# Kernel tuning notes

Hardware: AMD Instinct MI355X
Metric: run time of the kernel (lower is better)

## Reference

```python
import jax, jax.numpy as jnp
import numpy as np

B, S, D = 4, 2048, 768
H = 12
HD = D // H  # 64


def setup_inputs() -> dict:
    key = jax.random.key(0)
    k1, k2, k3 = jax.random.split(key, 3)
    x = jax.random.normal(k1, (B, S, D), dtype=jnp.float32)
    w_qkv = jax.random.normal(k2, (D, 3 * D), dtype=jnp.float32) * (1.0 / np.sqrt(D))
    b_qkv = jnp.zeros((3 * D,), dtype=jnp.float32)
    w_proj = jax.random.normal(k3, (D, D), dtype=jnp.float32) * (1.0 / np.sqrt(D))
    b_proj = jnp.zeros((D,), dtype=jnp.float32)
    return {"x": x, "w_qkv": w_qkv, "b_qkv": b_qkv, "w_proj": w_proj, "b_proj": b_proj}


def reference(x, w_qkv, b_qkv, w_proj, b_proj):
    b, s, d = x.shape
    qkv = x @ w_qkv + b_qkv                      # [B,S,3D]
    q, k, v = jnp.split(qkv, 3, axis=-1)
    # [B,S,D] -> [B,H,S,HD]
    q = q.reshape(b, s, H, HD).transpose(0, 2, 1, 3)
    k = k.reshape(b, s, H, HD).transpose(0, 2, 1, 3)
    v = v.reshape(b, s, H, HD).transpose(0, 2, 1, 3)
    scores = jnp.einsum("bhqd,bhkd->bhqk", q, k) / jnp.sqrt(jnp.float32(HD))
    causal = jnp.tril(jnp.ones((s, s), dtype=bool))
    scores = jnp.where(causal[None, None, :, :], scores, jnp.float32(-jnp.inf))
    attn = jax.nn.softmax(scores, axis=-1)       # dropout p=0.0 -> identity
    out = jnp.einsum("bhqk,bhkd->bhqd", attn, v)  # [B,H,S,HD]
    out = out.transpose(0, 2, 1, 3).reshape(b, s, d)
    return out @ w_proj + b_proj
```

## Files before the change

kernel.cpp:

```cpp
#include <hip/hip_runtime.h>
#include <hip/hip_bf16.h>

typedef __hip_bfloat16 bf16;
typedef __bf16 bf16x8 __attribute__((ext_vector_type(8)));
typedef float f32x4 __attribute__((ext_vector_type(4)));

#define MFMA(a, b, c) __builtin_amdgcn_mfma_f32_16x16x32_bf16(a, b, c, 0, 0, 0)
#define EXP2F(x) __builtin_exp2f(x)

constexpr int Bn = 4, Sn = 2048, Dn = 768, Hn = 12;
constexpr int N3 = 3 * Dn;
constexpr int Mrows = Bn * Sn;

constexpr size_t XB_OFF    = 0;
constexpr size_t WQKV_OFF  = 12582912;
constexpr size_t WPROJ_OFF = 16121856;
constexpr size_t Q_OFF     = 17301504;
constexpr size_t K_OFF     = 29884416;
constexpr size_t VT_OFF    = 42467328;
constexpr size_t O_OFF     = 55050240;

#define QSCALE 0.1803368801111243f

__device__ __forceinline__ void gload16(const void* g, void* l) {
  __builtin_amdgcn_global_load_lds((__attribute__((address_space(1))) void*)g,
                                   (__attribute__((address_space(3))) void*)l,
                                   16, 0, 0);
}

__device__ __forceinline__ unsigned int cvt_pk_bf16(float lo, float hi) {
  unsigned int r;
  asm("v_cvt_pk_bf16_f32 %0, %1, %2" : "=v"(r) : "v"(lo), "v"(hi));
  return r;
}

__global__ __launch_bounds__(256) void cvt_x_kernel(const float* __restrict__ in,
                                                    bf16* __restrict__ out, int n4) {
  int i = blockIdx.x * 256 + threadIdx.x;
  if (i >= n4) return;
  float4 f = reinterpret_cast<const float4*>(in)[i];
  uint2 o;
  o.x = cvt_pk_bf16(f.x, f.y);
  o.y = cvt_pk_bf16(f.z, f.w);
  reinterpret_cast<uint2*>(out)[i] = o;
}

__global__ __launch_bounds__(256) void transpose_cvt(const float* __restrict__ in,
                                                     bf16* __restrict__ out, int K, int N) {
  __shared__ float tile[32][33];
  int n0 = blockIdx.x * 32, k0 = blockIdx.y * 32;
  int tx = threadIdx.x & 31, ty = threadIdx.x >> 5;
  for (int r = ty; r < 32; r += 8)
    tile[r][tx] = in[(size_t)(k0 + r) * N + n0 + tx];
  __syncthreads();
  for (int r = ty; r < 32; r += 8)
    out[(size_t)(n0 + r) * K + k0 + tx] = __float2bfloat16(tile[tx][r]);
}

__global__ __launch_bounds__(256) void gemm_qkv(const bf16* __restrict__ A,
                                                const bf16* __restrict__ BT,
                                                const float* __restrict__ bias,
                                                bf16* __restrict__ Qo,
                                                bf16* __restrict__ Ko,
                                                bf16* __restrict__ Vt) {
  __shared__ __align__(16) bf16 As[2][128 * 32];
  __shared__ __align__(16) bf16 Bs[2][128 * 32];
  const int tid = threadIdx.x;
  const int m0 = blockIdx.x * 128, n0 = blockIdx.y * 128;
  const int w = tid >> 6, lane = tid & 63;
  const int wr = w >> 1, wc = w & 1;
  const int lr = lane & 15, lg = lane >> 4;

  f32x4 acc[4][4] = {};

  auto stage = [&](int k0, int sb) {
    for (int r = 0; r < 2; ++r) {
      int c = tid + r * 256;
      int row = c >> 2, ch = c & 3;
      int gch = ch ^ ((row >> 1) & 3);
      gload16(A + (size_t)(m0 + row) * Dn + k0 + gch * 8, &As[sb][c * 8]);
      gload16(BT + (size_t)(n0 + row) * Dn + k0 + gch * 8, &Bs[sb][c * 8]);
    }
  };

  stage(0, 0);
  __syncthreads();

  const int sw = (lr >> 1) & 3;
  const int aoff = (wr * 64 + lr) * 32 + ((lg ^ sw) << 3);
  const int boff = (wc * 64 + lr) * 32 + ((lg ^ sw) << 3);
  int buf = 0;

  for (int kt = 0; kt < 24; ++kt) {
    if (kt < 23) stage((kt + 1) * 32, buf ^ 1);
    bf16x8 af[4], bfr[4];
    for (int mi = 0; mi < 4; ++mi)
      af[mi] = *reinterpret_cast<const bf16x8*>(&As[buf][aoff + mi * 512]);
    for (int ni = 0; ni < 4; ++ni)
      bfr[ni] = *reinterpret_cast<const bf16x8*>(&Bs[buf][boff + ni * 512]);
    for (int mi = 0; mi < 4; ++mi)
      for (int ni = 0; ni < 4; ++ni)
        acc[mi][ni] = MFMA(af[mi], bfr[ni], acc[mi][ni]);
    __syncthreads();
    buf ^= 1;
  }

  for (int ni = 0; ni < 4; ++ni) {
    const int col = n0 + wc * 64 + ni * 16 + lr;
    const float bv = bias[col];
    const int seg = (col >= Dn) + (col >= 2 * Dn);
    const int d = col - seg * Dn;
    const int h = d >> 6, hd = d & 63;
    for (int mi = 0; mi < 4; ++mi) {
      f32x4 v = acc[mi][ni];
      const int row0 = m0 + wr * 64 + mi * 16 + lg * 4;
      const int b = row0 >> 11, s0 = row0 & 2047;
      const size_t bh = (size_t)(b * Hn + h);
      if (seg == 2) {
        uint2 pk;
        pk.x = cvt_pk_bf16(v[0] + bv, v[1] + bv);
        pk.y = cvt_pk_bf16(v[2] + bv, v[3] + bv);
        *reinterpret_cast<uint2*>(&Vt[(bh * 64 + hd) * Sn + s0]) = pk;
      } else if (seg == 0) {
        for (int r = 0; r < 4; ++r)
          Qo[(bh * Sn + s0 + r) * 64 + hd] = __float2bfloat16((v[r] + bv) * QSCALE);
      } else {
        for (int r = 0; r < 4; ++r)
          Ko[(bh * Sn + s0 + r) * 64 + hd] = __float2bfloat16(v[r] + bv);
      }
    }
  }
}

__global__ __launch_bounds__(256) void attn_fwd(const bf16* __restrict__ Q,
                                                const bf16* __restrict__ K,
                                                const bf16* __restrict__ Vt,
                                                bf16* __restrict__ O) {
  __shared__ __align__(16) bf16 Ks[2][64 * 64];
  __shared__ __align__(16) bf16 Vs[2][64 * 64];
  __shared__ __align__(16) bf16 Ps[4][16 * 64];
  const int tid = threadIdx.x, w = tid >> 6, lane = tid & 63;
  const int lr = lane & 15, lg = lane >> 4;
  const int bid = blockIdx.x;
  const int qt = 31 - (bid / 48);
  const int bh = bid % 48;
  const int q0 = qt * 64;
  const size_t base = (size_t)bh * Sn * 64;
  const int wrow = q0 + w * 16;

  bf16x8 qf[2];
  for (int kk = 0; kk < 2; ++kk)
    qf[kk] = *reinterpret_cast<const bf16x8*>(
        Q + base + (size_t)(wrow + lr) * 64 + kk * 32 + lg * 8);

  f32x4 o[4] = {};
  f32x4 lacc = {};

  const int nt = qt + 1;

  const int c0 = tid, c1 = tid + 256;
  const int r0 = c0 >> 3, s0w = (c0 & 7) ^ (r0 & 7);
  const int r1 = c1 >> 3, s1w = (c1 & 7) ^ (r1 & 7);
  const bf16* kp0 = K + base + r0 * 64 + s0w * 8;
  const bf16* kp1 = K + base + r1 * 64 + s1w * 8;
  const bf16* vp0 = Vt + base + (size_t)r0 * Sn + s0w * 8;
  const bf16* vp1 = Vt + base + (size_t)r1 * Sn + s1w * 8;

  gload16(kp0, &Ks[0][c0 * 8]);
  gload16(kp1, &Ks[0][c1 * 8]);
  gload16(vp0, &Vs[0][c0 * 8]);
  gload16(vp1, &Vs[0][c1 * 8]);
  kp0 += 4096; kp1 += 4096; vp0 += 64; vp1 += 64;
  __syncthreads();

  int buf = 0;
  for (int t = 0; t < nt; ++t) {
    if (t + 1 < nt) {
      const int sb = buf ^ 1;
      gload16(kp0, &Ks[sb][c0 * 8]);
      gload16(kp1, &Ks[sb][c1 * 8]);
      gload16(vp0, &Vs[sb][c0 * 8]);
      gload16(vp1, &Vs[sb][c1 * 8]);
      kp0 += 4096; kp1 += 4096; vp0 += 64; vp1 += 64;
    }

    f32x4 sf[4];
    __builtin_amdgcn_s_setprio(1);
    for (int ni = 0; ni < 4; ++ni) {
      const int krow = ni * 16 + lr;
      bf16x8 kf0 = *reinterpret_cast<const bf16x8*>(&Ks[buf][krow * 64 + (lg ^ (lr & 7)) * 8]);
      bf16x8 kf1 = *reinterpret_cast<const bf16x8*>(&Ks[buf][krow * 64 + ((4 + lg) ^ (lr & 7)) * 8]);
      f32x4 z = {};
      z = MFMA(kf0, qf[0], z);
      z = MFMA(kf1, qf[1], z);
      sf[ni] = z;
    }
    __builtin_amdgcn_s_setprio(0);
    if (t == nt - 1) {
      const int qg = wrow + lr;
      for (int ni = 0; ni < 4; ++ni)
        for (int r = 0; r < 4; ++r) {
          int kg = t * 64 + ni * 16 + lg * 4 + r;
          if (kg > qg) sf[ni][r] = -1e30f;
        }
    }
    for (int ni = 0; ni < 4; ++ni) {
      f32x4 z = sf[ni];
      z[0] = EXP2F(z[0]);
      z[1] = EXP2F(z[1]);
      z[2] = EXP2F(z[2]);
      z[3] = EXP2F(z[3]);
      sf[ni] = z;
      lacc += z;
    }
    for (int ni = 0; ni < 4; ++ni) {
      const int chunk = ni * 2 + (lg >> 1);
      const int eoff = lr * 64 + ((chunk ^ (lr & 7)) << 3) + ((lg & 1) << 2);
      uint2 pk;
      pk.x = cvt_pk_bf16(sf[ni][0], sf[ni][1]);
      pk.y = cvt_pk_bf16(sf[ni][2], sf[ni][3]);
      *reinterpret_cast<uint2*>(&Ps[w][eoff]) = pk;
    }
    asm volatile("s_waitcnt lgkmcnt(0)" ::: "memory");
    __builtin_amdgcn_sched_barrier(0);
    __builtin_amdgcn_s_setprio(1);
    for (int kk = 0; kk < 2; ++kk) {
      const int psw = ((kk * 4 + lg) ^ (lr & 7)) << 3;
      bf16x8 pf = *reinterpret_cast<const bf16x8*>(&Ps[w][lr * 64 + psw]);
      for (int di = 0; di < 4; ++di) {
        bf16x8 vf = *reinterpret_cast<const bf16x8*>(&Vs[buf][(di * 16 + lr) * 64 + psw]);
        o[di] = MFMA(vf, pf, o[di]);
      }
    }
    __builtin_amdgcn_s_setprio(0);
    __syncthreads();
    buf ^= 1;
  }

  float l = (lacc[0] + lacc[1]) + (lacc[2] + lacc[3]);
  l += __shfl_xor(l, 16);
  l += __shfl_xor(l, 32);
  const float inv = 1.0f / l;
  const int b = bh / Hn, h = bh % Hn;
  const size_t rowbase = ((size_t)b * Sn + wrow + lr) * Dn + h * 64;
  for (int di = 0; di < 4; ++di) {
    f32x4 ov = o[di];
    uint2 pk;
    pk.x = cvt_pk_bf16(ov[0] * inv, ov[1] * inv);
    pk.y = cvt_pk_bf16(ov[2] * inv, ov[3] * inv);
    *reinterpret_cast<uint2*>(&O[rowbase + di * 16 + lg * 4]) = pk;
  }
}

__global__ __launch_bounds__(256) void gemm_proj(const bf16* __restrict__ A,
                                                 const bf16* __restrict__ BT,
                                                 const float* __restrict__ bias,
                                                 float* __restrict__ out) {
  __shared__ __align__(16) bf16 As[2][128 * 32];
  __shared__ __align__(16) bf16 Bs[2][128 * 32];
  const int tid = threadIdx.x;
  const int m0 = blockIdx.x * 128, n0 = blockIdx.y * 128;
  const int w = tid >> 6, lane = tid & 63;
  const int wr = w >> 1, wc = w & 1;
  const int lr = lane & 15, lg = lane >> 4;

  f32x4 acc[4][4] = {};

  auto stage = [&](int k0, int sb) {
    for (int r = 0; r < 2; ++r) {
      int c = tid + r * 256;
      int row = c >> 2, ch = c & 3;
      int gch = ch ^ ((row >> 1) & 3);
      gload16(A + (size_t)(m0 + row) * Dn + k0 + gch * 8, &As[sb][c * 8]);
      gload16(BT + (size_t)(n0 + row) * Dn + k0 + gch * 8, &Bs[sb][c * 8]);
    }
  };

  stage(0, 0);
  __syncthreads();

  const int sw = (lr >> 1) & 3;
  const int aoff = (wr * 64 + lr) * 32 + ((lg ^ sw) << 3);
  const int boff = (wc * 64 + lr) * 32 + ((lg ^ sw) << 3);
  int buf = 0;

  for (int kt = 0; kt < 24; ++kt) {
    if (kt < 23) stage((kt + 1) * 32, buf ^ 1);
    bf16x8 af[4], bfr[4];
    for (int mi = 0; mi < 4; ++mi)
      af[mi] = *reinterpret_cast<const bf16x8*>(&As[buf][aoff + mi * 512]);
    for (int ni = 0; ni < 4; ++ni)
      bfr[ni] = *reinterpret_cast<const bf16x8*>(&Bs[buf][boff + ni * 512]);
    for (int mi = 0; mi < 4; ++mi)
      for (int ni = 0; ni < 4; ++ni)
        acc[mi][ni] = MFMA(af[mi], bfr[ni], acc[mi][ni]);
    __syncthreads();
    buf ^= 1;
  }

  for (int ni = 0; ni < 4; ++ni) {
    const int col = n0 + wc * 64 + ni * 16 + lr;
    const float bv = bias[col];
    for (int mi = 0; mi < 4; ++mi) {
      f32x4 v = acc[mi][ni];
      for (int r = 0; r < 4; ++r) {
        const int row = m0 + wr * 64 + mi * 16 + lg * 4 + r;
        out[(size_t)row * Dn + col] = v[r] + bv;
      }
    }
  }
}

extern "C" void kernel_launch(void* const* d_in, const int* in_sizes, int n_in,
                              void* d_out, int out_size, void* d_ws, size_t ws_size,
                              hipStream_t stream) {
  const float* x      = (const float*)d_in[0];
  const float* w_qkv  = (const float*)d_in[1];
  const float* b_qkv  = (const float*)d_in[2];
  const float* w_proj = (const float*)d_in[3];
  const float* b_proj = (const float*)d_in[4];
  float* out = (float*)d_out;

  char* ws = (char*)d_ws;
  bf16* xb     = (bf16*)(ws + XB_OFF);
  bf16* wqkvT  = (bf16*)(ws + WQKV_OFF);
  bf16* wprojT = (bf16*)(ws + WPROJ_OFF);
  bf16* Qb     = (bf16*)(ws + Q_OFF);
  bf16* Kb     = (bf16*)(ws + K_OFF);
  bf16* Vtb    = (bf16*)(ws + VT_OFF);
  bf16* Ob     = (bf16*)(ws + O_OFF);

  cvt_x_kernel<<<(Mrows * Dn / 4 + 255) / 256, 256, 0, stream>>>(x, xb, Mrows * Dn / 4);
  transpose_cvt<<<dim3(N3 / 32, Dn / 32), 256, 0, stream>>>(w_qkv, wqkvT, Dn, N3);
  transpose_cvt<<<dim3(Dn / 32, Dn / 32), 256, 0, stream>>>(w_proj, wprojT, Dn, Dn);
  gemm_qkv<<<dim3(Mrows / 128, N3 / 128), 256, 0, stream>>>(xb, wqkvT, b_qkv, Qb, Kb, Vtb);
  attn_fwd<<<32 * 48, 256, 0, stream>>>(Qb, Kb, Vtb, Ob);
  gemm_proj<<<dim3(Mrows / 128, Dn / 128), 256, 0, stream>>>(Ob, wprojT, b_proj, out);
}
```

Measured before the change: 144.4 us.

## Use 128-row query tiles with 8 waves per attention block

Doubles the attention block to 512 threads so each block processes 128 query rows and shares each K/V tile load across eight waves, halving global K/V traffic per query. Blocks are reordered in an interleaved big/small pattern to balance causal work across the grid. Waves whose rows lie entirely before a key tile skip compute, but they still wait at the barrier. The trade-off is coarser blocks and half as many of them, which can hurt occupancy and tail balance.

```diff
diff --git a/kernel.cpp b/kernel.cpp
--- a/kernel.cpp
+++ b/kernel.cpp
@@ -132,19 +132,20 @@
   }
 }
 
-__global__ __launch_bounds__(256) void attn_fwd(const bf16* __restrict__ Q,
+__global__ __launch_bounds__(512) void attn_fwd(const bf16* __restrict__ Q,
                                                 const bf16* __restrict__ K,
                                                 const bf16* __restrict__ Vt,
                                                 bf16* __restrict__ O) {
   __shared__ __align__(16) bf16 Ks[2][64 * 64];
   __shared__ __align__(16) bf16 Vs[2][64 * 64];
-  __shared__ __align__(16) bf16 Ps[4][16 * 64];
+  __shared__ __align__(16) bf16 Ps[8][16 * 64];
   const int tid = threadIdx.x, w = tid >> 6, lane = tid & 63;
   const int lr = lane & 15, lg = lane >> 4;
   const int bid = blockIdx.x;
-  const int qt = 31 - (bid / 48);
+  const int pt = bid / 48;
+  const int qt = (pt < 8) ? (15 - 2 * pt) : (2 * pt - 16);
   const int bh = bid % 48;
-  const int q0 = qt * 64;
+  const int q0 = qt * 128;
   const size_t base = (size_t)bh * Sn * 64;
   const int wrow = q0 + w * 16;
 
@@ -156,83 +157,77 @@
   f32x4 o[4] = {};
   f32x4 lacc = {};
 
-  const int nt = qt + 1;
-
-  const int c0 = tid, c1 = tid + 256;
-  const int r0 = c0 >> 3, s0w = (c0 & 7) ^ (r0 & 7);
-  const int r1 = c1 >> 3, s1w = (c1 & 7) ^ (r1 & 7);
-  const bf16* kp0 = K + base + r0 * 64 + s0w * 8;
-  const bf16* kp1 = K + base + r1 * 64 + s1w * 8;
-  const bf16* vp0 = Vt + base + (size_t)r0 * Sn + s0w * 8;
-  const bf16* vp1 = Vt + base + (size_t)r1 * Sn + s1w * 8;
-
-  gload16(kp0, &Ks[0][c0 * 8]);
-  gload16(kp1, &Ks[0][c1 * 8]);
-  gload16(vp0, &Vs[0][c0 * 8]);
-  gload16(vp1, &Vs[0][c1 * 8]);
-  kp0 += 4096; kp1 += 4096; vp0 += 64; vp1 += 64;
+  const int nt = 2 * qt + 2;
+
+  const int r0 = tid >> 3, s0w = (tid & 7) ^ (r0 & 7);
+  const bf16* kp = K + base + r0 * 64 + s0w * 8;
+  const bf16* vp = Vt + base + (size_t)r0 * Sn + s0w * 8;
+
+  gload16(kp, &Ks[0][tid * 8]);
+  gload16(vp, &Vs[0][tid * 8]);
+  kp += 4096; vp += 64;
   __syncthreads();
 
   int buf = 0;
   for (int t = 0; t < nt; ++t) {
     if (t + 1 < nt) {
       const int sb = buf ^ 1;
-      gload16(kp0, &Ks[sb][c0 * 8]);
-      gload16(kp1, &Ks[sb][c1 * 8]);
-      gload16(vp0, &Vs[sb][c0 * 8]);
-      gload16(vp1, &Vs[sb][c1 * 8]);
-      kp0 += 4096; kp1 += 4096; vp0 += 64; vp1 += 64;
-    }
-
-    f32x4 sf[4];
-    __builtin_amdgcn_s_setprio(1);
-    for (int ni = 0; ni < 4; ++ni) {
-      const int krow = ni * 16 + lr;
-      bf16x8 kf0 = *reinterpret_cast<const bf16x8*>(&Ks[buf][krow * 64 + (lg ^ (lr & 7)) * 8]);
-      bf16x8 kf1 = *reinterpret_cast<const bf16x8*>(&Ks[buf][krow * 64 + ((4 + lg) ^ (lr & 7)) * 8]);
-      f32x4 z = {};
-      z = MFMA(kf0, qf[0], z);
-      z = MFMA(kf1, qf[1], z);
-      sf[ni] = z;
-    }
-    __builtin_amdgcn_s_setprio(0);
-    if (t == nt - 1) {
-      const int qg = wrow + lr;
-      for (int ni = 0; ni < 4; ++ni)
-        for (int r = 0; r < 4; ++r) {
-          int kg = t * 64 + ni * 16 + lg * 4 + r;
-          if (kg > qg) sf[ni][r] = -1e30f;
+      gload16(kp, &Ks[sb][tid * 8]);
+      gload16(vp, &Vs[sb][tid * 8]);
+      kp += 4096; vp += 64;
+    }
+
+    if (t * 64 <= wrow + 15) {
+      f32x4 sf[4];
+      __builtin_amdgcn_s_setprio(1);
+      for (int ni = 0; ni < 4; ++ni) {
+        const int krow = ni * 16 + lr;
+        bf16x8 kf0 = *reinterpret_cast<const bf16x8*>(&Ks[buf][krow * 64 + (lg ^ (lr & 7)) * 8]);
+        bf16x8 kf1 = *reinterpret_cast<const bf16x8*>(&Ks[buf][krow * 64 + ((4 + lg) ^ (lr & 7)) * 8]);
+        f32x4 z = {};
+        z = MFMA(kf0, qf[0], z);
+        z = MFMA(kf1, qf[1], z);
+        sf[ni] = z;
+      }
+      __builtin_amdgcn_s_setprio(0);
+      if (t * 64 + 63 > wrow) {
+        const int qg = wrow + lr;
+        for (int ni = 0; ni < 4; ++ni)
+          for (int r = 0; r < 4; ++r) {
+            int kg = t * 64 + ni * 16 + lg * 4 + r;
+            if (kg > qg) sf[ni][r] = -1e30f;
+          }
+      }
+      for (int ni = 0; ni < 4; ++ni) {
+        f32x4 z = sf[ni];
+        z[0] = EXP2F(z[0]);
+        z[1] = EXP2F(z[1]);
+        z[2] = EXP2F(z[2]);
+        z[3] = EXP2F(z[3]);
+        sf[ni] = z;
+        lacc += z;
+      }
+      for (int ni = 0; ni < 4; ++ni) {
+        const int chunk = ni * 2 + (lg >> 1);
+        const int eoff = lr * 64 + ((chunk ^ (lr & 7)) << 3) + ((lg & 1) << 2);
+        uint2 pk;
+        pk.x = cvt_pk_bf16(sf[ni][0], sf[ni][1]);
+        pk.y = cvt_pk_bf16(sf[ni][2], sf[ni][3]);
+        *reinterpret_cast<uint2*>(&Ps[w][eoff]) = pk;
+      }
+      asm volatile("s_waitcnt lgkmcnt(0)" ::: "memory");
+      __builtin_amdgcn_sched_barrier(0);
+      __builtin_amdgcn_s_setprio(1);
+      for (int kk = 0; kk < 2; ++kk) {
+        const int psw = ((kk * 4 + lg) ^ (lr & 7)) << 3;
+        bf16x8 pf = *reinterpret_cast<const bf16x8*>(&Ps[w][lr * 64 + psw]);
+        for (int di = 0; di < 4; ++di) {
+          bf16x8 vf = *reinterpret_cast<const bf16x8*>(&Vs[buf][(di * 16 + lr) * 64 + psw]);
+          o[di] = MFMA(vf, pf, o[di]);
         }
-    }
-    for (int ni = 0; ni < 4; ++ni) {
-      f32x4 z = sf[ni];
-      z[0] = EXP2F(z[0]);
-      z[1] = EXP2F(z[1]);
-      z[2] = EXP2F(z[2]);
-      z[3] = EXP2F(z[3]);
-      sf[ni] = z;
-      lacc += z;
-    }
-    for (int ni = 0; ni < 4; ++ni) {
-      const int chunk = ni * 2 + (lg >> 1);
-      const int eoff = lr * 64 + ((chunk ^ (lr & 7)) << 3) + ((lg & 1) << 2);
-      uint2 pk;
-      pk.x = cvt_pk_bf16(sf[ni][0], sf[ni][1]);
-      pk.y = cvt_pk_bf16(sf[ni][2], sf[ni][3]);
-      *reinterpret_cast<uint2*>(&Ps[w][eoff]) = pk;
-    }
-    asm volatile("s_waitcnt lgkmcnt(0)" ::: "memory");
-    __builtin_amdgcn_sched_barrier(0);
-    __builtin_amdgcn_s_setprio(1);
-    for (int kk = 0; kk < 2; ++kk) {
-      const int psw = ((kk * 4 + lg) ^ (lr & 7)) << 3;
-      bf16x8 pf = *reinterpret_cast<const bf16x8*>(&Ps[w][lr * 64 + psw]);
-      for (int di = 0; di < 4; ++di) {
-        bf16x8 vf = *reinterpret_cast<const bf16x8*>(&Vs[buf][(di * 16 + lr) * 64 + psw]);
-        o[di] = MFMA(vf, pf, o[di]);
-      }
-    }
-    __builtin_amdgcn_s_setprio(0);
+      }
+      __builtin_amdgcn_s_setprio(0);
+    }
     __syncthreads();
     buf ^= 1;
   }
@@ -334,6 +329,6 @@
   transpose_cvt<<<dim3(N3 / 32, Dn / 32), 256, 0, stream>>>(w_qkv, wqkvT, Dn, N3);
   transpose_cvt<<<dim3(Dn / 32, Dn / 32), 256, 0, stream>>>(w_proj, wprojT, Dn, Dn);
   gemm_qkv<<<dim3(Mrows / 128, N3 / 128), 256, 0, stream>>>(xb, wqkvT, b_qkv, Qb, Kb, Vtb);
-  attn_fwd<<<32 * 48, 256, 0, stream>>>(Qb, Kb, Vtb, Ob);
+  attn_fwd<<<768, 512, 0, stream>>>(Qb, Kb, Vtb, Ob);
   gemm_proj<<<dim3(Mrows / 128, Dn / 128), 256, 0, stream>>>(Ob, wprojT, b_proj, out);
 }
```

New measurement: 160.7 us. +11.3%, slower.

## Load V fragments directly from global into registers instead of LDS

Applied to the files above, without the earlier changes.

V tiles are no longer staged through double-buffered shared memory. Each wave now reads its V^T MFMA operand fragments straight from global memory at the top of every iteration, and the PV MFMAs consume them from registers. This removes the LDS writes and reads for V and halves the LDS footprint, which may allow more blocks per CU. The cost is that all four waves redundantly fetch the same V data from global/L2, and those loads have no prefetch distance beyond the QK^T compute that sits between issue and use.

```diff
diff --git a/kernel.cpp b/kernel.cpp
--- a/kernel.cpp
+++ b/kernel.cpp
@@ -137,7 +137,6 @@
                                                 const bf16* __restrict__ Vt,
                                                 bf16* __restrict__ O) {
   __shared__ __align__(16) bf16 Ks[2][64 * 64];
-  __shared__ __align__(16) bf16 Vs[2][64 * 64];
   __shared__ __align__(16) bf16 Ps[4][16 * 64];
   const int tid = threadIdx.x, w = tid >> 6, lane = tid & 63;
   const int lr = lane & 15, lg = lane >> 4;
@@ -163,25 +162,34 @@
   const int r1 = c1 >> 3, s1w = (c1 & 7) ^ (r1 & 7);
   const bf16* kp0 = K + base + r0 * 64 + s0w * 8;
   const bf16* kp1 = K + base + r1 * 64 + s1w * 8;
-  const bf16* vp0 = Vt + base + (size_t)r0 * Sn + s0w * 8;
-  const bf16* vp1 = Vt + base + (size_t)r1 * Sn + s1w * 8;
+
+  const bf16* vrow0 = Vt + base + (size_t)(lr) * Sn + lg * 8;
+  const bf16* vrow1 = vrow0 + (size_t)16 * Sn;
+  const bf16* vrow2 = vrow0 + (size_t)32 * Sn;
+  const bf16* vrow3 = vrow0 + (size_t)48 * Sn;
 
   gload16(kp0, &Ks[0][c0 * 8]);
   gload16(kp1, &Ks[0][c1 * 8]);
-  gload16(vp0, &Vs[0][c0 * 8]);
-  gload16(vp1, &Vs[0][c1 * 8]);
-  kp0 += 4096; kp1 += 4096; vp0 += 64; vp1 += 64;
+  kp0 += 4096; kp1 += 4096;
   __syncthreads();
 
   int buf = 0;
   for (int t = 0; t < nt; ++t) {
+    bf16x8 vf00 = *reinterpret_cast<const bf16x8*>(vrow0);
+    bf16x8 vf01 = *reinterpret_cast<const bf16x8*>(vrow0 + 32);
+    bf16x8 vf10 = *reinterpret_cast<const bf16x8*>(vrow1);
+    bf16x8 vf11 = *reinterpret_cast<const bf16x8*>(vrow1 + 32);
+    bf16x8 vf20 = *reinterpret_cast<const bf16x8*>(vrow2);
+    bf16x8 vf21 = *reinterpret_cast<const bf16x8*>(vrow2 + 32);
+    bf16x8 vf30 = *reinterpret_cast<const bf16x8*>(vrow3);
+    bf16x8 vf31 = *reinterpret_cast<const bf16x8*>(vrow3 + 32);
+    vrow0 += 64; vrow1 += 64; vrow2 += 64; vrow3 += 64;
+
     if (t + 1 < nt) {
       const int sb = buf ^ 1;
       gload16(kp0, &Ks[sb][c0 * 8]);
       gload16(kp1, &Ks[sb][c1 * 8]);
-      gload16(vp0, &Vs[sb][c0 * 8]);
-      gload16(vp1, &Vs[sb][c1 * 8]);
-      kp0 += 4096; kp1 += 4096; vp0 += 64; vp1 += 64;
+      kp0 += 4096; kp1 += 4096;
     }
 
     f32x4 sf[4];
@@ -224,13 +232,19 @@
     asm volatile("s_waitcnt lgkmcnt(0)" ::: "memory");
     __builtin_amdgcn_sched_barrier(0);
     __builtin_amdgcn_s_setprio(1);
-    for (int kk = 0; kk < 2; ++kk) {
-      const int psw = ((kk * 4 + lg) ^ (lr & 7)) << 3;
-      bf16x8 pf = *reinterpret_cast<const bf16x8*>(&Ps[w][lr * 64 + psw]);
-      for (int di = 0; di < 4; ++di) {
-        bf16x8 vf = *reinterpret_cast<const bf16x8*>(&Vs[buf][(di * 16 + lr) * 64 + psw]);
-        o[di] = MFMA(vf, pf, o[di]);
-      }
+    {
+      const int psw0 = (lg ^ (lr & 7)) << 3;
+      const int psw1 = ((4 + lg) ^ (lr & 7)) << 3;
+      bf16x8 pf0 = *reinterpret_cast<const bf16x8*>(&Ps[w][lr * 64 + psw0]);
+      bf16x8 pf1 = *reinterpret_cast<const bf16x8*>(&Ps[w][lr * 64 + psw1]);
+      o[0] = MFMA(vf00, pf0, o[0]);
+      o[1] = MFMA(vf10, pf0, o[1]);
+      o[2] = MFMA(vf20, pf0, o[2]);
+      o[3] = MFMA(vf30, pf0, o[3]);
+      o[0] = MFMA(vf01, pf1, o[0]);
+      o[1] = MFMA(vf11, pf1, o[1]);
+      o[2] = MFMA(vf21, pf1, o[2]);
+      o[3] = MFMA(vf31, pf1, o[3]);
     }
     __builtin_amdgcn_s_setprio(0);
     __syncthreads();
```

Result: slower. 193.8 us (+34.2%).
